# Kernel tuning notes

Hardware: AMD Instinct MI355X
Metric: run time of the kernel (lower is better)

The kernel has to match this reference:

```python
import jax, jax.numpy as jnp
import numpy as np

N_NODES = 50000
N_EDGES = 800000
DIMS = [100, 512, 256, 128, 200]  # input -> conv1 -> conv2 -> conv3 -> conv4


def setup_inputs() -> dict:
    key = jax.random.key(0)
    ks = jax.random.split(key, 2 + 4)
    x = jax.random.normal(ks[0], (N_NODES, DIMS[0]), dtype=jnp.float32)
    edge_index = jax.random.randint(ks[1], (2, N_EDGES), 0, N_NODES, dtype=jnp.int64)
    inp = {"x": x, "edge_index": edge_index}
    for i in range(4):
        fan_in = DIMS[i]
        W = jax.random.normal(ks[2 + i], (DIMS[i], DIMS[i + 1]), dtype=jnp.float32) * (1.0 / np.sqrt(fan_in)).astype(np.float32)
        b = jnp.zeros((DIMS[i + 1],), dtype=jnp.float32)
        inp[f"W{i + 1}"] = W
        inp[f"b{i + 1}"] = b
    return inp


def _gcn_layer(x, row, col, norm, W, b, n):
    # PyG GCNConv: linear transform first, then normalized scatter-add, then bias.
    h = x @ W                           # [N, out]
    msg = h[row] * norm[:, None]        # [E+N, out] gather + edge scale
    agg = jax.ops.segment_sum(msg, col, num_segments=n)  # scatter-add to targets
    return agg + b


def reference(x, edge_index, W1, b1, W2, b2, W3, b3, W4, b4):
    n = x.shape[0]
    loop = jnp.arange(n, dtype=edge_index.dtype)
    row = jnp.concatenate([edge_index[0], loop])  # sources (with self-loops)
    col = jnp.concatenate([edge_index[1], loop])  # targets (with self-loops)
    deg = jax.ops.segment_sum(jnp.ones_like(col, dtype=x.dtype), col, num_segments=n)
    dinv = jnp.where(deg > 0, jax.lax.rsqrt(deg), 0.0)
    norm = dinv[row] * dinv[col]  # symmetric D^{-1/2}(A+I)D^{-1/2} edge weights

    out = jax.nn.relu(_gcn_layer(x, row, col, norm, W1, b1, n))
    out = jax.nn.relu(_gcn_layer(out, row, col, norm, W2, b2, n))
    out = jax.nn.relu(_gcn_layer(out, row, col, norm, W3, b3, n))
    out = jax.nn.relu(_gcn_layer(out, row, col, norm, W4, b4, n))
    return jnp.mean(out, axis=0, keepdims=True)  # [1, 200]
```

## Files before the change

### kernel.cpp

```cpp
#include <hip/hip_runtime.h>
#include <hip/hip_bf16.h>


#define NN 50000
#define NE 800000
#define PRANGE (NN / 8)
#define CAP 64

typedef __attribute__((ext_vector_type(8))) _Float16 f16x8;
typedef __attribute__((ext_vector_type(4))) float floatx4;
typedef __attribute__((ext_vector_type(2))) float floatx2;

union U16x8 {
    uint4 u4;
    f16x8 h;
    _Float16 e[8];
};

__device__ __forceinline__ void dec16(const unsigned char* p, float* f) {
    uint4 v = *(const uint4*)p;
    unsigned w[4] = {v.x, v.y, v.z, v.w};
#pragma unroll
    for (int k = 0; k < 4; k++) {
        floatx2 lo = __builtin_amdgcn_cvt_pk_f32_fp8(w[k], false);
        floatx2 hi = __builtin_amdgcn_cvt_pk_f32_fp8(w[k], true);
        f[k * 4 + 0] = lo[0];
        f[k * 4 + 1] = lo[1];
        f[k * 4 + 2] = hi[0];
        f[k * 4 + 3] = hi[1];
    }
}

__device__ __forceinline__ uint4 enc16(const float* f) {
    uint4 r;
    unsigned w;
    w = __builtin_amdgcn_cvt_pk_fp8_f32(f[0], f[1], 0, false);
    w = __builtin_amdgcn_cvt_pk_fp8_f32(f[2], f[3], (int)w, true);
    r.x = w;
    w = __builtin_amdgcn_cvt_pk_fp8_f32(f[4], f[5], 0, false);
    w = __builtin_amdgcn_cvt_pk_fp8_f32(f[6], f[7], (int)w, true);
    r.y = w;
    w = __builtin_amdgcn_cvt_pk_fp8_f32(f[8], f[9], 0, false);
    w = __builtin_amdgcn_cvt_pk_fp8_f32(f[10], f[11], (int)w, true);
    r.z = w;
    w = __builtin_amdgcn_cvt_pk_fp8_f32(f[12], f[13], 0, false);
    w = __builtin_amdgcn_cvt_pk_fp8_f32(f[14], f[15], (int)w, true);
    r.w = w;
    return r;
}

__device__ __forceinline__ uint4 dec8_f16(uint2 v) {
    floatx2 f0 = __builtin_amdgcn_cvt_pk_f32_fp8(v.x, false);
    floatx2 f1 = __builtin_amdgcn_cvt_pk_f32_fp8(v.x, true);
    floatx2 f2 = __builtin_amdgcn_cvt_pk_f32_fp8(v.y, false);
    floatx2 f3 = __builtin_amdgcn_cvt_pk_f32_fp8(v.y, true);
    U16x8 o;
    o.e[0] = (_Float16)f0[0]; o.e[1] = (_Float16)f0[1];
    o.e[2] = (_Float16)f1[0]; o.e[3] = (_Float16)f1[1];
    o.e[4] = (_Float16)f2[0]; o.e[5] = (_Float16)f2[1];
    o.e[6] = (_Float16)f3[0]; o.e[7] = (_Float16)f3[1];
    return o.u4;
}

__global__ __launch_bounds__(256) void setup_kernel(
    const void* __restrict__ ei, unsigned* __restrict__ fillc,
    float* __restrict__ out, int* __restrict__ r32, int* __restrict__ c32,
    const float* __restrict__ x, unsigned char* __restrict__ xb,
    const float* __restrict__ W1, const float* __restrict__ W2,
    const float* __restrict__ W3, const float* __restrict__ W4,
    _Float16* __restrict__ w1t, _Float16* __restrict__ w2t,
    _Float16* __restrict__ w3t, _Float16* __restrict__ w4t) {
    int bx = blockIdx.x, t = threadIdx.x;
    if (bx < 196) {
        int tid = bx * 256 + t;
        if (tid < NN) fillc[tid] = 0u;
        if (bx == 0 && t < 200) out[t] = 0.f;
        return;
    }
    if (bx < 196 + 3125) {
        int e = (bx - 196) * 256 + t;
        __shared__ int nz;
        if (t == 0) nz = 0;
        __syncthreads();
        unsigned w = ((const unsigned*)ei)[2 * (size_t)e + 1];
        if (w) atomicOr(&nz, 1);
        __syncthreads();
        int r, c;
        if (nz == 0) {
            r = (int)((const long long*)ei)[e];
            c = (int)((const long long*)ei)[NE + e];
        } else {
            r = ((const int*)ei)[e];
            c = ((const int*)ei)[NE + e];
        }
        r32[e] = r;
        c32[e] = c;
        return;
    }
    if (bx < 196 + 3125 + 1563) {
        int tid = (bx - 196 - 3125) * 256 + t;
        int node = tid >> 3, sub = tid & 7;
        if (node >= NN) return;
        int base = sub * 16;
        float f[16];
#pragma unroll
        for (int i = 0; i < 16; i++) {
            int cc = base + i;
            f[i] = (cc < 100) ? x[(size_t)node * 100 + cc] : 0.f;
        }
        *(uint4*)(xb + (size_t)node * 128 + base) = enc16(f);
        return;
    }
    int b = bx - 196 - 3125 - 1563;
    const float* W;
    _Float16* Wt;
    int K, N, Kpad, tid;
    if (b < 256)      { W = W1; Wt = w1t; K = 100; N = 512; Kpad = 128; tid = b * 256 + t; }
    else if (b < 768) { W = W2; Wt = w2t; K = 512; N = 256; Kpad = 512; tid = (b - 256) * 256 + t; }
    else if (b < 896) { W = W3; Wt = w3t; K = 256; N = 128; Kpad = 256; tid = (b - 768) * 256 + t; }
    else              { W = W4; Wt = w4t; K = 128; N = 200; Kpad = 128; tid = (b - 896) * 256 + t; }
    int n = tid / Kpad, k = tid - n * Kpad;
    float v = (k < K && n < N) ? W[(size_t)k * N + n] : 0.f;
    Wt[tid] = (_Float16)v;
}

__global__ __launch_bounds__(256) void fill_kernel(
    const int* __restrict__ r32, const int* __restrict__ c32,
    unsigned* __restrict__ fillc, int* __restrict__ ep) {
    const int part = blockIdx.x & 7;
    const int lo = part * PRANGE, hi = lo + PRANGE;
    const int group = blockIdx.x >> 3;
    const int base = (group * 256 + threadIdx.x) * 4;
    if (base >= NE) return;
    int4 c4 = *(const int4*)(c32 + base);
    int4 r4 = *(const int4*)(r32 + base);
    int c[4] = {c4.x, c4.y, c4.z, c4.w};
    int r[4] = {r4.x, r4.y, r4.z, r4.w};
    int pos[4];
#pragma unroll
    for (int i = 0; i < 4; i++) {
        pos[i] = -1;
        if (c[i] >= lo && c[i] < hi) {
            int idx = (int)atomicAdd(&fillc[c[i]], 1u);
            if (idx < CAP) pos[i] = c[i] * CAP + idx;
        }
    }
#pragma unroll
    for (int i = 0; i < 4; i++)
        if (pos[i] >= 0) ep[pos[i]] = r[i];
}

template <int D, int BR>
__global__ __launch_bounds__(256) void agg_kernel(
    const unsigned char* __restrict__ H, const int* __restrict__ ep,
    const unsigned* __restrict__ fillc, const float* __restrict__ bias,
    unsigned char* __restrict__ O) {
    constexpr int LPN = D / 16;
    int tid = blockIdx.x * 256 + threadIdx.x;
    int node = tid / LPN;
    int sub = tid % LPN;
    if (node >= NN) return;
    int deg = (int)fillc[node];
    if (deg > CAP) deg = CAP;
    const int s = node * CAP;
    const int e = s + deg;
    float dc = rsqrtf((float)(deg + 1));
    float selfw = dc * dc;
    const int base = sub * 16;
    const unsigned char* __restrict__ Hb = H + base;
    float acc[16], t0[16], t1[16];
    dec16(Hb + (size_t)node * D, t0);
#pragma unroll
    for (int i = 0; i < 16; i++) acc[i] = selfw * t0[i];
    int j = s;
    for (; j + 2 <= e; j += 2) {
        int r0 = ep[j];
        int r1 = ep[j + 1];
        float w0 = rsqrtf((float)((int)fillc[r0] + 1)) * dc;
        float w1 = rsqrtf((float)((int)fillc[r1] + 1)) * dc;
        dec16(Hb + (size_t)r0 * D, t0);
        dec16(Hb + (size_t)r1 * D, t1);
#pragma unroll
        for (int i = 0; i < 16; i++) acc[i] = fmaf(w0, t0[i], acc[i]);
#pragma unroll
        for (int i = 0; i < 16; i++) acc[i] = fmaf(w1, t1[i], acc[i]);
    }
    if (j < e) {
        int r0 = ep[j];
        float w0 = rsqrtf((float)((int)fillc[r0] + 1)) * dc;
        dec16(Hb + (size_t)r0 * D, t0);
#pragma unroll
        for (int i = 0; i < 16; i++) acc[i] = fmaf(w0, t0[i], acc[i]);
    }
    if (BR) {
#pragma unroll
        for (int i = 0; i < 16; i++) acc[i] = fmaxf(acc[i] + bias[base + i], 0.f);
    }
    *(uint4*)(O + (size_t)node * D + base) = enc16(acc);
}

template <int EPI>
__global__ __launch_bounds__(256) void gemm_kernel(
    const unsigned char* __restrict__ A, const _Float16* __restrict__ B,
    const float* __restrict__ bias, unsigned char* __restrict__ Cb,
    float* __restrict__ outmean, int M, int K, int N) {
    __shared__ _Float16 Asl[64 * 36];
    __shared__ _Float16 Bsl[128 * 36];
    __shared__ float red[128];
    const int m0 = blockIdx.y * 64;
    const int n0 = blockIdx.x * 128;
    const int t = threadIdx.x;
    const int lane = t & 63, w = t >> 6;
    const int wm = (w >> 1) * 32, wn = (w & 1) * 64;
    const int r16 = lane & 15, quad = lane >> 4;

    const int arow = t >> 2, ac8 = (t & 3) * 8;
    int gma = m0 + arow; if (gma > M - 1) gma = M - 1;
    const unsigned char* Aptr = A + (size_t)gma * K + ac8;
    const int rb0 = t >> 2, kb0 = (t & 3) * 8;
    const int rb1 = (t + 256) >> 2, kb1 = kb0;
    const _Float16* Bptr0 = B + (size_t)(n0 + rb0) * K + kb0;
    const _Float16* Bptr1 = B + (size_t)(n0 + rb1) * K + kb1;

    floatx4 acc[2][4];
    const floatx4 fz = {0.f, 0.f, 0.f, 0.f};
#pragma unroll
    for (int i = 0; i < 2; i++)
#pragma unroll
        for (int j = 0; j < 4; j++) acc[i][j] = fz;

    uint2 apf = *(const uint2*)Aptr;
    uint4 bpf0 = *(const uint4*)Bptr0;
    uint4 bpf1 = *(const uint4*)Bptr1;

    for (int kc = 0; kc < K; kc += 32) {
        __syncthreads();
        *(uint4*)(Asl + arow * 36 + ac8) = dec8_f16(apf);
        *(uint4*)(Bsl + rb0 * 36 + kb0) = bpf0;
        *(uint4*)(Bsl + rb1 * 36 + kb1) = bpf1;
        __syncthreads();
        if (kc + 32 < K) {
            apf = *(const uint2*)(Aptr + kc + 32);
            bpf0 = *(const uint4*)(Bptr0 + kc + 32);
            bpf1 = *(const uint4*)(Bptr1 + kc + 32);
        }
        f16x8 af[2], bf[4];
#pragma unroll
        for (int i = 0; i < 2; i++)
            af[i] = *(const f16x8*)(Asl + (wm + i * 16 + r16) * 36 + quad * 8);
#pragma unroll
        for (int j = 0; j < 4; j++)
            bf[j] = *(const f16x8*)(Bsl + (wn + j * 16 + r16) * 36 + quad * 8);
#pragma unroll
        for (int i = 0; i < 2; i++)
#pragma unroll
            for (int j = 0; j < 4; j++)
                acc[i][j] = __builtin_amdgcn_mfma_f32_16x16x32_f16(af[i], bf[j], acc[i][j], 0, 0, 0);
    }

    if (EPI == 2) {
        if (t < 128) red[t] = 0.f;
        __syncthreads();
#pragma unroll
        for (int j = 0; j < 4; j++) {
            int col = n0 + wn + j * 16 + r16;
            float s = 0.f;
            if (col < N) {
                float bv = bias[col];
#pragma unroll
                for (int i = 0; i < 2; i++) {
                    int mbase = m0 + wm + i * 16 + quad * 4;
#pragma unroll
                    for (int r = 0; r < 4; r++)
                        if (mbase + r < M) s += fmaxf(acc[i][j][r] + bv, 0.f);
                }
            }
            atomicAdd(&red[wn + j * 16 + r16], s);
        }
        __syncthreads();
        if (t < 128) {
            int col = n0 + t;
            if (col < N) atomicAdd(outmean + col, red[t] * (1.0f / (float)NN));
        }
    } else {
#pragma unroll
        for (int i = 0; i < 2; i++) {
            int mbase = m0 + wm + i * 16 + quad * 4;
#pragma unroll
            for (int r = 0; r < 4; r++) {
                int m = mbase + r;
                if (m >= M) continue;
#pragma unroll
                for (int j = 0; j < 4; j++) {
                    int col = n0 + wn + j * 16 + r16;
                    float v = acc[i][j][r];
                    if (EPI == 1) v = fmaxf(v + bias[col], 0.f);
                    unsigned pk = __builtin_amdgcn_cvt_pk_fp8_f32(v, v, 0, false);
                    Cb[(size_t)m * N + col] = (unsigned char)(pk & 0xffu);
                }
            }
        }
    }
}

extern "C" void kernel_launch(void* const* d_in, const int* in_sizes, int n_in,
                              void* d_out, int out_size, void* d_ws, size_t ws_size,
                              hipStream_t stream) {
    const float* x  = (const float*)d_in[0];
    const void*  ei = d_in[1];
    const float* W1 = (const float*)d_in[2];
    const float* b1 = (const float*)d_in[3];
    const float* W2 = (const float*)d_in[4];
    const float* b2 = (const float*)d_in[5];
    const float* W3 = (const float*)d_in[6];
    const float* b3 = (const float*)d_in[7];
    const float* W4 = (const float*)d_in[8];
    const float* b4 = (const float*)d_in[9];
    float* out = (float*)d_out;

    char* ws = (char*)d_ws;
    size_t o = 0;
    auto alloc = [&](size_t bytes) -> void* {
        void* p = ws + o;
        o += (bytes + 255) & ~(size_t)255;
        return p;
    };
    unsigned* fillc = (unsigned*)alloc((size_t)NN * 4);
    int*      r32   = (int*)alloc((size_t)NE * 4);
    int*      c32   = (int*)alloc((size_t)NE * 4);
    int*      ep    = (int*)alloc((size_t)NN * CAP * 4);
    _Float16* w1t = (_Float16*)alloc((size_t)512 * 128 * 2);
    _Float16* w2t = (_Float16*)alloc((size_t)256 * 512 * 2);
    _Float16* w3t = (_Float16*)alloc((size_t)128 * 256 * 2);
    _Float16* w4t = (_Float16*)alloc((size_t)256 * 128 * 2);
    unsigned char* xb  = (unsigned char*)alloc((size_t)NN * 128);
    unsigned char* A1b = (unsigned char*)alloc((size_t)NN * 128);
    unsigned char* H1b = (unsigned char*)alloc((size_t)NN * 512);
    unsigned char* t2b = (unsigned char*)alloc((size_t)NN * 256);
    unsigned char* H2b = (unsigned char*)alloc((size_t)NN * 256);
    unsigned char* t3b = (unsigned char*)alloc((size_t)NN * 128);
    unsigned char* h3b = (unsigned char*)alloc((size_t)NN * 128);
    unsigned char* A4b = (unsigned char*)alloc((size_t)NN * 128);

    setup_kernel<<<196 + 3125 + 1563 + 1024, 256, 0, stream>>>(
        ei, fillc, out, r32, c32, x, xb, W1, W2, W3, W4, w1t, w2t, w3t, w4t);
    fill_kernel<<<782 * 8, 256, 0, stream>>>(r32, c32, fillc, ep);

    const int MB64 = (NN + 63) / 64;
    const int AB128 = (NN * 8 + 255) / 256;
    const int AB256 = (NN * 16 + 255) / 256;

    agg_kernel<128, 0><<<AB128, 256, 0, stream>>>(xb, ep, fillc, nullptr, A1b);
    gemm_kernel<1><<<dim3(4, MB64), 256, 0, stream>>>(A1b, w1t, b1, H1b, nullptr, NN, 128, 512);
    gemm_kernel<0><<<dim3(2, MB64), 256, 0, stream>>>(H1b, w2t, nullptr, t2b, nullptr, NN, 512, 256);
    agg_kernel<256, 1><<<AB256, 256, 0, stream>>>(t2b, ep, fillc, b2, H2b);
    gemm_kernel<0><<<dim3(1, MB64), 256, 0, stream>>>(H2b, w3t, nullptr, t3b, nullptr, NN, 256, 128);
    agg_kernel<128, 1><<<AB128, 256, 0, stream>>>(t3b, ep, fillc, b3, h3b);
    agg_kernel<128, 0><<<AB128, 256, 0, stream>>>(h3b, ep, fillc, nullptr, A4b);
    gemm_kernel<2><<<dim3(2, MB64), 256, 0, stream>>>(A4b, w4t, b4, nullptr, out, NN, 128, 200);
}
```

Baseline: 315.2 us.

## Factor symmetric GCN normalization into per-node pre/post scaling of features

Rewrites the D^-1/2 (A+I) D^-1/2 aggregation so source-side scaling happens on the producer side (the GEMM epilogue or previous aggregation output multiplies rows by dinv). The aggregation then becomes a plain unweighted sum followed by one dinv multiply. This removes the per-edge random fillc lookup and rsqrt in the gather loop for three aggregations. It also changes where the degree is clamped, now using the true degree for dc, and stores pre-scaled fp8 values, which may shift quantization error.

```diff
diff --git a/kernel.cpp b/kernel.cpp
--- a/kernel.cpp
+++ b/kernel.cpp
@@ -150,7 +150,7 @@
         if (pos[i] >= 0) ep[pos[i]] = r[i];
 }
 
-template <int D, int BR>
+template <int D, int BR, int PS, int SS>
 __global__ __launch_bounds__(256) void agg_kernel(
     const unsigned char* __restrict__ H, const int* __restrict__ ep,
     const unsigned* __restrict__ fillc, const float* __restrict__ bias,
@@ -160,50 +160,79 @@
     int node = tid / LPN;
     int sub = tid % LPN;
     if (node >= NN) return;
-    int deg = (int)fillc[node];
-    if (deg > CAP) deg = CAP;
+    int degt = (int)fillc[node];
+    int deg = degt > CAP ? CAP : degt;
     const int s = node * CAP;
     const int e = s + deg;
-    float dc = rsqrtf((float)(deg + 1));
-    float selfw = dc * dc;
+    float dc = rsqrtf((float)(degt + 1));
     const int base = sub * 16;
     const unsigned char* __restrict__ Hb = H + base;
     float acc[16], t0[16], t1[16];
     dec16(Hb + (size_t)node * D, t0);
-#pragma unroll
-    for (int i = 0; i < 16; i++) acc[i] = selfw * t0[i];
-    int j = s;
-    for (; j + 2 <= e; j += 2) {
-        int r0 = ep[j];
-        int r1 = ep[j + 1];
-        float w0 = rsqrtf((float)((int)fillc[r0] + 1)) * dc;
-        float w1 = rsqrtf((float)((int)fillc[r1] + 1)) * dc;
-        dec16(Hb + (size_t)r0 * D, t0);
-        dec16(Hb + (size_t)r1 * D, t1);
-#pragma unroll
-        for (int i = 0; i < 16; i++) acc[i] = fmaf(w0, t0[i], acc[i]);
-#pragma unroll
-        for (int i = 0; i < 16; i++) acc[i] = fmaf(w1, t1[i], acc[i]);
-    }
-    if (j < e) {
-        int r0 = ep[j];
-        float w0 = rsqrtf((float)((int)fillc[r0] + 1)) * dc;
-        dec16(Hb + (size_t)r0 * D, t0);
-#pragma unroll
-        for (int i = 0; i < 16; i++) acc[i] = fmaf(w0, t0[i], acc[i]);
+    if (SS) {
+#pragma unroll
+        for (int i = 0; i < 16; i++) acc[i] = t0[i];
+        int j = s;
+        for (; j + 2 <= e; j += 2) {
+            int r0 = ep[j];
+            int r1 = ep[j + 1];
+            dec16(Hb + (size_t)r0 * D, t0);
+            dec16(Hb + (size_t)r1 * D, t1);
+#pragma unroll
+            for (int i = 0; i < 16; i++) acc[i] += t0[i];
+#pragma unroll
+            for (int i = 0; i < 16; i++) acc[i] += t1[i];
+        }
+        if (j < e) {
+            int r0 = ep[j];
+            dec16(Hb + (size_t)r0 * D, t0);
+#pragma unroll
+            for (int i = 0; i < 16; i++) acc[i] += t0[i];
+        }
+#pragma unroll
+        for (int i = 0; i < 16; i++) acc[i] *= dc;
+    } else {
+        float selfw = dc * dc;
+#pragma unroll
+        for (int i = 0; i < 16; i++) acc[i] = selfw * t0[i];
+        int j = s;
+        for (; j + 2 <= e; j += 2) {
+            int r0 = ep[j];
+            int r1 = ep[j + 1];
+            float w0 = rsqrtf((float)((int)fillc[r0] + 1)) * dc;
+            float w1 = rsqrtf((float)((int)fillc[r1] + 1)) * dc;
+            dec16(Hb + (size_t)r0 * D, t0);
+            dec16(Hb + (size_t)r1 * D, t1);
+#pragma unroll
+            for (int i = 0; i < 16; i++) acc[i] = fmaf(w0, t0[i], acc[i]);
+#pragma unroll
+            for (int i = 0; i < 16; i++) acc[i] = fmaf(w1, t1[i], acc[i]);
+        }
+        if (j < e) {
+            int r0 = ep[j];
+            float w0 = rsqrtf((float)((int)fillc[r0] + 1)) * dc;
+            dec16(Hb + (size_t)r0 * D, t0);
+#pragma unroll
+            for (int i = 0; i < 16; i++) acc[i] = fmaf(w0, t0[i], acc[i]);
+        }
     }
     if (BR) {
 #pragma unroll
         for (int i = 0; i < 16; i++) acc[i] = fmaxf(acc[i] + bias[base + i], 0.f);
     }
+    if (PS) {
+#pragma unroll
+        for (int i = 0; i < 16; i++) acc[i] *= dc;
+    }
     *(uint4*)(O + (size_t)node * D + base) = enc16(acc);
 }
 
-template <int EPI>
+template <int EPI, int PS>
 __global__ __launch_bounds__(256) void gemm_kernel(
     const unsigned char* __restrict__ A, const _Float16* __restrict__ B,
-    const float* __restrict__ bias, unsigned char* __restrict__ Cb,
-    float* __restrict__ outmean, int M, int K, int N) {
+    const float* __restrict__ bias, const unsigned* __restrict__ fillc,
+    unsigned char* __restrict__ Cb, float* __restrict__ outmean,
+    int M, int K, int N) {
     __shared__ _Float16 Asl[64 * 36];
     __shared__ _Float16 Bsl[128 * 36];
     __shared__ float red[128];
@@ -290,11 +319,14 @@
             for (int r = 0; r < 4; r++) {
                 int m = mbase + r;
                 if (m >= M) continue;
+                float dsc = 1.f;
+                if (PS) dsc = rsqrtf((float)((int)fillc[m] + 1));
 #pragma unroll
                 for (int j = 0; j < 4; j++) {
                     int col = n0 + wn + j * 16 + r16;
                     float v = acc[i][j][r];
                     if (EPI == 1) v = fmaxf(v + bias[col], 0.f);
+                    if (PS) v *= dsc;
                     unsigned pk = __builtin_amdgcn_cvt_pk_fp8_f32(v, v, 0, false);
                     Cb[(size_t)m * N + col] = (unsigned char)(pk & 0xffu);
                 }
@@ -350,12 +382,12 @@
     const int AB128 = (NN * 8 + 255) / 256;
     const int AB256 = (NN * 16 + 255) / 256;
 
-    agg_kernel<128, 0><<<AB128, 256, 0, stream>>>(xb, ep, fillc, nullptr, A1b);
-    gemm_kernel<1><<<dim3(4, MB64), 256, 0, stream>>>(A1b, w1t, b1, H1b, nullptr, NN, 128, 512);
-    gemm_kernel<0><<<dim3(2, MB64), 256, 0, stream>>>(H1b, w2t, nullptr, t2b, nullptr, NN, 512, 256);
-    agg_kernel<256, 1><<<AB256, 256, 0, stream>>>(t2b, ep, fillc, b2, H2b);
-    gemm_kernel<0><<<dim3(1, MB64), 256, 0, stream>>>(H2b, w3t, nullptr, t3b, nullptr, NN, 256, 128);
-    agg_kernel<128, 1><<<AB128, 256, 0, stream>>>(t3b, ep, fillc, b3, h3b);
-    agg_kernel<128, 0><<<AB128, 256, 0, stream>>>(h3b, ep, fillc, nullptr, A4b);
-    gemm_kernel<2><<<dim3(2, MB64), 256, 0, stream>>>(A4b, w4t, b4, nullptr, out, NN, 128, 200);
-}
+    agg_kernel<128, 0, 0, 0><<<AB128, 256, 0, stream>>>(xb, ep, fillc, nullptr, A1b);
+    gemm_kernel<1, 0><<<dim3(4, MB64), 256, 0, stream>>>(A1b, w1t, b1, fillc, H1b, nullptr, NN, 128, 512);
+    gemm_kernel<0, 1><<<dim3(2, MB64), 256, 0, stream>>>(H1b, w2t, nullptr, fillc, t2b, nullptr, NN, 512, 256);
+    agg_kernel<256, 1, 0, 1><<<AB256, 256, 0, stream>>>(t2b, ep, fillc, b2, H2b);
+    gemm_kernel<0, 1><<<dim3(1, MB64), 256, 0, stream>>>(H2b, w3t, nullptr, fillc, t3b, nullptr, NN, 256, 128);
+    agg_kernel<128, 1, 1, 1><<<AB128, 256, 0, stream>>>(t3b, ep, fillc, b3, h3b);
+    agg_kernel<128, 0, 0, 1><<<AB128, 256, 0, stream>>>(h3b, ep, fillc, nullptr, A4b);
+    gemm_kernel<2, 0><<<dim3(2, MB64), 256, 0, stream>>>(A4b, w4t, b4, fillc, nullptr, out, NN, 128, 200);
+}
```

After: 312.6 us. Within noise of the previous version (-0.8%).
